# Optimization experiments

Measured on AMD Instinct MI355X. Metric: run time of the kernel, lower is better.

The kernel has to match this reference:

```python
import jax, jax.numpy as jnp
import numpy as np

TEMPERATURE = 0.1
BASE_TEMPERATURE = 0.07
N = 8192
D = 128


def setup_inputs() -> dict:
    key = jax.random.key(0)
    kf, kl = jax.random.split(key)
    feats = jax.random.normal(kf, (N, 1, D), dtype=jnp.float32)
    # contrastive embeddings are typically L2-normalized upstream
    feats = feats / jnp.linalg.norm(feats, axis=-1, keepdims=True)
    labels = jax.random.randint(kl, (N,), 0, 2, dtype=jnp.int32)
    return {"feats": feats, "labels": labels}


def reference(feats, labels):
    # feats: [anchor_num, n_view=1, D]; labels: [anchor_num] binary fg/bg
    anchor_num, n_view, d = feats.shape
    n = anchor_num * n_view  # n_view == 1 in this module
    contrast_feature = feats.reshape(n, d)

    lab = labels.reshape(-1, 1)
    pos_mask = (lab == lab.T).astype(feats.dtype)  # [N, N]
    neg_mask = 1.0 - pos_mask

    # [N, N] similarity logits
    logits = jnp.matmul(contrast_feature, contrast_feature.T) / TEMPERATURE
    logits_max = jax.lax.stop_gradient(jnp.max(logits, axis=1, keepdims=True))
    logits = logits - logits_max

    # mask out self-contrast on the diagonal (logits_mask in torch code)
    idx = jnp.arange(n)
    pos_mask = pos_mask.at[idx, idx].set(0.0)

    exp_logits = jnp.exp(logits)
    neg_logits = jnp.sum(exp_logits * neg_mask, axis=1, keepdims=True)  # [N,1]
    log_prob = logits - jnp.log(exp_logits + neg_logits)

    mean_log_prob_pos = jnp.sum(pos_mask * log_prob, axis=1) / jnp.sum(pos_mask, axis=1)
    loss = -(TEMPERATURE / BASE_TEMPERATURE) * mean_log_prob_pos
    return jnp.mean(loss)
```

## Files before the change

kernel.cpp:

```cpp
#include <hip/hip_runtime.h>
#include <hip/hip_bf16.h>

#define NN 8192
#define DD 128

typedef short bf16x8 __attribute__((ext_vector_type(8)));
typedef float f32x4 __attribute__((ext_vector_type(4)));

#define LOG2E 1.4426950408889634f
#define K2f   14.426950408889634f

#define M_OFF    (NN * DD * 2)
#define LABF_OFF (M_OFF + NN * 4)
#define G_OFF    (LABF_OFF + NN * 4)
#define CNT_OFF  (G_OFF + 256 * 4)
#define EG_OFF   (CNT_OFF + 256)
#define ELG_OFF  (EG_OFF + NN * 4)

__device__ __forceinline__ unsigned short f2bf(float x) {
    unsigned u = __float_as_uint(x);
    u = (u + 0x7FFFu + ((u >> 16) & 1u)) >> 16;
    return (unsigned short)u;
}

__global__ __launch_bounds__(256) void prep_kernel(const float* __restrict__ F,
        const int* __restrict__ labels, unsigned short* __restrict__ P,
        float* __restrict__ M, float* __restrict__ labf, float* __restrict__ G,
        int* __restrict__ cnt1, float* __restrict__ Eg, float* __restrict__ Elg) {
    __shared__ float sG[256];
    __shared__ int scnt;
    const int tid = threadIdx.x;
    sG[tid] = 0.f;
    if (tid == 0) scnt = 0;
    __syncthreads();
    const int wave = tid >> 6, lane = tid & 63;
    const int half = lane >> 5, l32 = lane & 31;
    const int rb = blockIdx.x * 32;
    if (tid < 32) { Eg[rb + tid] = 0.f; Elg[rb + tid] = 0.f; }
    int mycnt = 0;
    float g1a[4] = {0.f, 0.f, 0.f, 0.f}, gta[4] = {0.f, 0.f, 0.f, 0.f};
    const int ch = l32 >> 1, hh = l32 & 1;
    #pragma unroll
    for (int it = 0; it < 4; ++it) {
        const int row = rb + it * 8 + wave * 2 + half;
        const int lab = labels[row];
        const float lf = (float)lab;
        const float4 f = *reinterpret_cast<const float4*>(F + row * DD + l32 * 4);
        ushort4 u;
        u.x = f2bf(f.x); u.y = f2bf(f.y); u.z = f2bf(f.z); u.w = f2bf(f.w);
        *reinterpret_cast<ushort4*>(P + ((size_t)ch * NN + row) * 8 + hh * 4) = u;
        g1a[0] = fmaf(lf, f.x, g1a[0]); gta[0] += f.x;
        g1a[1] = fmaf(lf, f.y, g1a[1]); gta[1] += f.y;
        g1a[2] = fmaf(lf, f.z, g1a[2]); gta[2] += f.z;
        g1a[3] = fmaf(lf, f.w, g1a[3]); gta[3] += f.w;
        float ss = fmaf(f.x, f.x, fmaf(f.y, f.y, fmaf(f.z, f.z, f.w * f.w)));
        #pragma unroll
        for (int off = 1; off < 32; off <<= 1) ss += __shfl_xor(ss, off);
        if (l32 == 0) {
            M[row] = 10.0f * ss;
            labf[row] = lf;
            mycnt += lab;
        }
    }
    #pragma unroll
    for (int j = 0; j < 4; ++j) {
        atomicAdd(&sG[l32 * 4 + j], g1a[j]);
        atomicAdd(&sG[128 + l32 * 4 + j], gta[j]);
    }
    if (l32 == 0 && mycnt) atomicAdd(&scnt, mycnt);
    __syncthreads();
    atomicAdd(&G[tid], sG[tid]);
    if (tid == 0) atomicAdd(cnt1, scnt);
}

__global__ __launch_bounds__(512, 4) void loss_kernel(
        const unsigned short* __restrict__ P, const float* __restrict__ M,
        const float* __restrict__ labf, float* __restrict__ Eg,
        float* __restrict__ Elg) {
    const int tid  = threadIdx.x;
    const int wave = tid >> 6, lane = tid & 63;
    const int quad = lane >> 4, l16 = lane & 15;
    const int rb = (blockIdx.x & 31) * 256;
    const int cb = (blockIdx.x >> 5) * 512;
    const int rw = rb + wave * 32;

    bf16x8 a[2][4];
    #pragma unroll
    for (int m = 0; m < 2; m++)
        #pragma unroll
        for (int kb = 0; kb < 4; kb++)
            a[m][kb] = *reinterpret_cast<const bf16x8*>(
                P + ((size_t)(kb * 4 + quad) * NN + rw + m * 16 + l16) * 8);

    float mneg[2][4];
    #pragma unroll
    for (int m = 0; m < 2; m++)
        #pragma unroll
        for (int r = 0; r < 4; r++)
            mneg[m][r] = -M[rw + m * 16 + quad * 4 + r] * LOG2E;

    const unsigned short* pB = P + ((size_t)quad * NN + cb + l16) * 8;
    const float* pL = labf + cb + l16;

    bf16x8 bb[2][4];
    #pragma unroll
    for (int kb = 0; kb < 4; kb++)
        bb[0][kb] = *reinterpret_cast<const bf16x8*>(pB + (size_t)kb * 4 * NN * 8);
    float lcur = pL[0];

    float accE[2][4] = {}, accEl[2][4] = {};

    #pragma unroll 4
    for (int it = 0; it < 32; ++it) {
        const int cur = it & 1, nxt = cur ^ 1;
        const int itn = (it + 1) & 31;
        #pragma unroll
        for (int kb = 0; kb < 4; kb++)
            bb[nxt][kb] = *reinterpret_cast<const bf16x8*>(
                pB + (size_t)kb * 4 * NN * 8 + itn * 128);
        const float lnxt = pL[itn * 16];

        f32x4 d0 = {0.f, 0.f, 0.f, 0.f}, d1 = {0.f, 0.f, 0.f, 0.f};
        #pragma unroll
        for (int kb = 0; kb < 4; kb++) {
            d0 = __builtin_amdgcn_mfma_f32_16x16x32_bf16(a[0][kb], bb[cur][kb], d0, 0, 0, 0);
            d1 = __builtin_amdgcn_mfma_f32_16x16x32_bf16(a[1][kb], bb[cur][kb], d1, 0, 0, 0);
        }

        #pragma unroll
        for (int m = 0; m < 2; m++) {
            #pragma unroll
            for (int r = 0; r < 4; r++) {
                const float vv = (m == 0) ? d0[r] : d1[r];
                const float e = exp2f(fmaf(vv, K2f, mneg[m][r]));
                accE[m][r] += e;
                accEl[m][r] = fmaf(lcur, e, accEl[m][r]);
            }
        }
        lcur = lnxt;
    }

    #pragma unroll
    for (int m = 0; m < 2; m++) {
        #pragma unroll
        for (int r = 0; r < 4; r++) {
            float e = accE[m][r], el = accEl[m][r];
            #pragma unroll
            for (int off = 1; off < 16; off <<= 1) {
                e  += __shfl_xor(e,  off);
                el += __shfl_xor(el, off);
            }
            if (l16 == 0) {
                const int row = rw + m * 16 + quad * 4 + r;
                atomicAdd(&Eg[row], e);
                atomicAdd(&Elg[row], el);
            }
        }
    }
}

__global__ __launch_bounds__(256) void final_kernel(
        const float* __restrict__ F, const float* __restrict__ M,
        const int* __restrict__ labels, const float* __restrict__ G,
        const int* __restrict__ cnt1, const float* __restrict__ Eg,
        const float* __restrict__ Elg, float* __restrict__ out) {
    __shared__ float sG[256];
    __shared__ float wsum[4];
    const int tid = threadIdx.x;
    sG[tid] = G[tid];
    __syncthreads();
    const int row = blockIdx.x * 256 + tid;
    const int lr = labels[row];
    float dot = 0.f;
    const float* f = F + (size_t)row * DD;
    #pragma unroll
    for (int k = 0; k < DD; k += 4) {
        const float4 fv = *reinterpret_cast<const float4*>(f + k);
        #pragma unroll
        for (int j = 0; j < 4; j++) {
            const float fj = (&fv.x)[j];
            const float g1 = sG[k + j];
            const float gl = lr ? g1 : (sG[128 + k + j] - g1);
            dot = fmaf(fj, gl, dot);
        }
    }
    const float E    = Eg[row];
    const float El   = Elg[row];
    const float Epos = lr ? El : (E - El);
    const float Si   = E - Epos;
    const float mi   = M[row];
    const int   c1   = *cnt1;
    const float cntp1 = (float)(lr ? c1 : (NN - c1));
    const float cnt   = cntp1 - 1.f;
    const float sum_l   = fmaf(10.f, dot, -cntp1 * mi);
    const float sum_log = cntp1 * __logf(Si) + Epos / Si;
    float li = -(10.f / 7.f) * (sum_l - sum_log) / cnt;
    #pragma unroll
    for (int off = 1; off < 64; off <<= 1) li += __shfl_xor(li, off);
    if ((tid & 63) == 0) wsum[tid >> 6] = li;
    __syncthreads();
    if (tid == 0)
        atomicAdd(out, (wsum[0] + wsum[1] + wsum[2] + wsum[3]) * (1.0f / NN));
}

extern "C" void kernel_launch(void* const* d_in, const int* in_sizes, int n_in,
                              void* d_out, int out_size, void* d_ws, size_t ws_size,
                              hipStream_t stream) {
    const float* F      = (const float*)d_in[0];
    const int*   labels = (const int*)d_in[1];
    float*       out    = (float*)d_out;
    char*        ws     = (char*)d_ws;
    unsigned short* P   = (unsigned short*)ws;
    float*       M      = (float*)(ws + M_OFF);
    float*       labf   = (float*)(ws + LABF_OFF);
    float*       G      = (float*)(ws + G_OFF);
    int*         cnt1   = (int*)(ws + CNT_OFF);
    float*       Eg     = (float*)(ws + EG_OFF);
    float*       Elg    = (float*)(ws + ELG_OFF);

    hipMemsetAsync(out, 0, sizeof(float), stream);
    hipMemsetAsync(ws + G_OFF, 0, 256 * 4 + 256, stream);

    prep_kernel<<<NN / 32, 256, 0, stream>>>(F, labels, P, M, labf, G, cnt1, Eg, Elg);
    loss_kernel<<<512, 512, 0, stream>>>(P, M, labf, Eg, Elg);
    final_kernel<<<NN / 256, 256, 0, stream>>>(F, M, labels, G, cnt1, Eg, Elg, out);
}
```

Before: 110.3 us.

## Exploit Gram matrix symmetry to compute only upper-triangular tiles

```diff
diff --git a/kernel.cpp b/kernel.cpp
--- a/kernel.cpp
+++ b/kernel.cpp
@@ -16,6 +16,8 @@
 #define CNT_OFF  (G_OFF + 256 * 4)
 #define EG_OFF   (CNT_OFF + 256)
 #define ELG_OFF  (EG_OFF + NN * 4)
+#define TEG_OFF  (ELG_OFF + NN * 4)
+#define TELG_OFF (TEG_OFF + NN * 4)
 
 __device__ __forceinline__ unsigned short f2bf(float x) {
     unsigned u = __float_as_uint(x);
@@ -26,7 +28,8 @@
 __global__ __launch_bounds__(256) void prep_kernel(const float* __restrict__ F,
         const int* __restrict__ labels, unsigned short* __restrict__ P,
         float* __restrict__ M, float* __restrict__ labf, float* __restrict__ G,
-        int* __restrict__ cnt1, float* __restrict__ Eg, float* __restrict__ Elg) {
+        int* __restrict__ cnt1, float* __restrict__ Eg, float* __restrict__ Elg,
+        float* __restrict__ TEg, float* __restrict__ TElg) {
     __shared__ float sG[256];
     __shared__ int scnt;
     const int tid = threadIdx.x;
@@ -36,7 +39,10 @@
     const int wave = tid >> 6, lane = tid & 63;
     const int half = lane >> 5, l32 = lane & 31;
     const int rb = blockIdx.x * 32;
-    if (tid < 32) { Eg[rb + tid] = 0.f; Elg[rb + tid] = 0.f; }
+    if (tid < 32) {
+        Eg[rb + tid] = 0.f; Elg[rb + tid] = 0.f;
+        TEg[rb + tid] = 0.f; TElg[rb + tid] = 0.f;
+    }
     int mycnt = 0;
     float g1a[4] = {0.f, 0.f, 0.f, 0.f}, gta[4] = {0.f, 0.f, 0.f, 0.f};
     const int ch = l32 >> 1, hh = l32 & 1;
@@ -76,13 +82,21 @@
 __global__ __launch_bounds__(512, 4) void loss_kernel(
         const unsigned short* __restrict__ P, const float* __restrict__ M,
         const float* __restrict__ labf, float* __restrict__ Eg,
-        float* __restrict__ Elg) {
+        float* __restrict__ Elg, float* __restrict__ TEg,
+        float* __restrict__ TElg) {
+    __shared__ float colE[256], colEl[256];
     const int tid  = threadIdx.x;
     const int wave = tid >> 6, lane = tid & 63;
     const int quad = lane >> 4, l16 = lane & 15;
-    const int rb = (blockIdx.x & 31) * 256;
-    const int cb = (blockIdx.x >> 5) * 512;
+
+    int b = blockIdx.x, rg = 0;
+    while (b >= 32 - rg) { b -= 32 - rg; rg++; }
+    const int cg = rg + b;
+    const bool diag = (b == 0);
+    const int rb = rg * 256, cb = cg * 256;
     const int rw = rb + wave * 32;
+
+    if (tid < 256) colE[tid] = 0.f; else colEl[tid - 256] = 0.f;
 
     bf16x8 a[2][4];
     #pragma unroll
@@ -92,12 +106,17 @@
             a[m][kb] = *reinterpret_cast<const bf16x8*>(
                 P + ((size_t)(kb * 4 + quad) * NN + rw + m * 16 + l16) * 8);
 
-    float mneg[2][4];
+    float mneg[2][4], w[2][4], lw[2][4];
     #pragma unroll
     for (int m = 0; m < 2; m++)
         #pragma unroll
-        for (int r = 0; r < 4; r++)
-            mneg[m][r] = -M[rw + m * 16 + quad * 4 + r] * LOG2E;
+        for (int r = 0; r < 4; r++) {
+            const int row = rw + m * 16 + quad * 4 + r;
+            const float mi = M[row];
+            mneg[m][r] = -mi * LOG2E;
+            w[m][r] = exp2f((mi - 10.f) * LOG2E);
+            lw[m][r] = labf[row] * w[m][r];
+        }
 
     const unsigned short* pB = P + ((size_t)quad * NN + cb + l16) * 8;
     const float* pL = labf + cb + l16;
@@ -109,11 +128,12 @@
     float lcur = pL[0];
 
     float accE[2][4] = {}, accEl[2][4] = {};
-
-    #pragma unroll 4
-    for (int it = 0; it < 32; ++it) {
+    __syncthreads();
+
+    #pragma unroll 2
+    for (int it = 0; it < 16; ++it) {
         const int cur = it & 1, nxt = cur ^ 1;
-        const int itn = (it + 1) & 31;
+        const int itn = (it + 1) & 15;
         #pragma unroll
         for (int kb = 0; kb < 4; kb++)
             bb[nxt][kb] = *reinterpret_cast<const bf16x8*>(
@@ -127,6 +147,7 @@
             d1 = __builtin_amdgcn_mfma_f32_16x16x32_bf16(a[1][kb], bb[cur][kb], d1, 0, 0, 0);
         }
 
+        float cE = 0.f, cEl = 0.f;
         #pragma unroll
         for (int m = 0; m < 2; m++) {
             #pragma unroll
@@ -135,6 +156,16 @@
                 const float e = exp2f(fmaf(vv, K2f, mneg[m][r]));
                 accE[m][r] += e;
                 accEl[m][r] = fmaf(lcur, e, accEl[m][r]);
+                cE  = fmaf(w[m][r],  e, cE);
+                cEl = fmaf(lw[m][r], e, cEl);
+            }
+        }
+        if (!diag) {
+            cE  += __shfl_xor(cE, 16);  cE  += __shfl_xor(cE, 32);
+            cEl += __shfl_xor(cEl, 16); cEl += __shfl_xor(cEl, 32);
+            if (quad == 0) {
+                atomicAdd(&colE[it * 16 + l16], cE);
+                atomicAdd(&colEl[it * 16 + l16], cEl);
             }
         }
         lcur = lnxt;
@@ -157,13 +188,20 @@
             }
         }
     }
+
+    if (!diag) {
+        __syncthreads();
+        if (tid < 256) atomicAdd(&TEg[cb + tid], colE[tid]);
+        else           atomicAdd(&TElg[cb + tid - 256], colEl[tid - 256]);
+    }
 }
 
 __global__ __launch_bounds__(256) void final_kernel(
         const float* __restrict__ F, const float* __restrict__ M,
         const int* __restrict__ labels, const float* __restrict__ G,
         const int* __restrict__ cnt1, const float* __restrict__ Eg,
-        const float* __restrict__ Elg, float* __restrict__ out) {
+        const float* __restrict__ Elg, const float* __restrict__ TEg,
+        const float* __restrict__ TElg, float* __restrict__ out) {
     __shared__ float sG[256];
     __shared__ float wsum[4];
     const int tid = threadIdx.x;
@@ -184,11 +222,12 @@
             dot = fmaf(fj, gl, dot);
         }
     }
-    const float E    = Eg[row];
-    const float El   = Elg[row];
+    const float mi = M[row];
+    const float tf = exp2f((10.f - mi) * LOG2E);
+    const float E    = Eg[row]  + tf * TEg[row];
+    const float El   = Elg[row] + tf * TElg[row];
     const float Epos = lr ? El : (E - El);
     const float Si   = E - Epos;
-    const float mi   = M[row];
     const int   c1   = *cnt1;
     const float cntp1 = (float)(lr ? c1 : (NN - c1));
     const float cnt   = cntp1 - 1.f;
@@ -217,11 +256,15 @@
     int*         cnt1   = (int*)(ws + CNT_OFF);
     float*       Eg     = (float*)(ws + EG_OFF);
     float*       Elg    = (float*)(ws + ELG_OFF);
+    float*       TEg    = (float*)(ws + TEG_OFF);
+    float*       TElg   = (float*)(ws + TELG_OFF);
 
     hipMemsetAsync(out, 0, sizeof(float), stream);
     hipMemsetAsync(ws + G_OFF, 0, 256 * 4 + 256, stream);
 
-    prep_kernel<<<NN / 32, 256, 0, stream>>>(F, labels, P, M, labf, G, cnt1, Eg, Elg);
-    loss_kernel<<<512, 512, 0, stream>>>(P, M, labf, Eg, Elg);
-    final_kernel<<<NN / 256, 256, 0, stream>>>(F, M, labels, G, cnt1, Eg, Elg, out);
-}
+    prep_kernel<<<NN / 32, 256, 0, stream>>>(F, labels, P, M, labf, G, cnt1,
+                                             Eg, Elg, TEg, TElg);
+    loss_kernel<<<528, 512, 0, stream>>>(P, M, labf, Eg, Elg, TEg, TElg);
+    final_kernel<<<NN / 256, 256, 0, stream>>>(F, M, labels, G, cnt1,
+                                               Eg, Elg, TEg, TElg, out);
+}
```

Result: no change. 108.6 us (-1.5%).
